# Performance work log

Measured on AMD Instinct MI355X. Metric: run time of the kernel, lower is better.

## Reference

```python
import jax, jax.numpy as jnp
import numpy as np

N = 4096      # nodes
E = 65536     # edges (avg degree 16)
NNIN = 64; NEIN = 64; NOPEN = 128; NHID = 128; NCLOSE = 128; NLAYER = 4
H = 0.1; NUM_OUT = 1024; LIN_HID = 256; EPS = 1e-5


def ln_all(x):
    # F.layer_norm(x, x.shape): normalize over ALL elements, no affine
    m = jnp.mean(x)
    v = jnp.mean((x - m) ** 2)
    return (x - m) * jax.lax.rsqrt(v + EPS)


def double_layer(x, K1, K2):
    # edgeConv with 2-D kernel == 1x1 conv == channel mixing
    x = jnp.einsum('oc,bcn->bon', K1, x)
    x = jnp.tanh(ln_all(x))
    return jnp.einsum('oc,bcn->bon', K2, x)


def node_grad(x, I, J, w):      # [1,C,N] -> [1,C,E]
    return w * (x[:, :, I] - x[:, :, J])


def node_ave(x, I, J, w):
    return 0.5 * w * (x[:, :, I] + x[:, :, J])


def edge_div(g, I, J, w, n):    # [1,C,E] -> [1,C,N], signed scatter-add
    wg = w * g
    z = jnp.zeros(g.shape[:2] + (n,), g.dtype)
    return z.at[:, :, I].add(wg).at[:, :, J].add(-wg)


def edge_ave(g, I, J, w, n):    # method='ave'
    wg = w * g
    z = jnp.zeros(g.shape[:2] + (n,), g.dtype)
    return 0.5 * (z.at[:, :, I].add(wg) + z.at[:, :, J].add(wg))


def setup_inputs():
    key = jax.random.key(0)
    ks = jax.random.split(key, 20)
    stdv = 1e-3
    nfeat = 3 * NOPEN  # varlet=False
    return {
        'xn': jax.random.normal(ks[0], (1, NNIN, N), jnp.float32),
        'xe': jax.random.normal(ks[1], (1, NEIN, E), jnp.float32),
        'iInd': jax.random.randint(ks[2], (E,), 0, N),
        'jInd': jax.random.randint(ks[3], (E,), 0, N),
        'K1Nopen': jax.random.normal(ks[4], (NOPEN, NNIN)) * stdv,
        'K2Nopen': jax.random.normal(ks[5], (NOPEN, NOPEN)) * stdv,
        'K1Eopen': jax.random.normal(ks[6], (NOPEN, NEIN)) * stdv,
        'K2Eopen': jax.random.normal(ks[7], (NOPEN, NOPEN)) * stdv,
        'KNclose': jax.random.normal(ks[8], (NCLOSE, NOPEN)) * stdv,
        'KE1': jax.random.uniform(ks[9], (NLAYER, NHID, nfeat)) * stdv,
        'KE2': jax.random.uniform(ks[10], (NLAYER, NOPEN, NHID)) * stdv,
        'KN1': jax.random.uniform(ks[11], (NLAYER, NHID, nfeat)) * stdv,
        'KN2': jax.random.uniform(ks[12], (NLAYER, NOPEN, NHID)) * stdv,
        'W1': jax.random.normal(ks[13], (LIN_HID, NCLOSE)) * 0.02,
        'b1': jnp.zeros((LIN_HID,), jnp.float32),
        'W2': jax.random.normal(ks[14], (NUM_OUT, LIN_HID)) * 0.02,
        'b2': jnp.zeros((NUM_OUT,), jnp.float32),
    }


def reference(xn, xe, iInd, jInd, K1Nopen, K2Nopen, K1Eopen, K2Eopen, KNclose,
              KE1, KE2, KN1, KN2, W1, b1, W2, b2):
    xn = double_layer(xn, K1Nopen, K2Nopen)
    xe = double_layer(xe, K1Eopen, K2Eopen)
    for i in range(NLAYER):
        # periodic pairwise-distance graph reweighting (cdist-style)
        f = xn[0]                                    # [C, N]
        s = jnp.sum(f * f, axis=0)                   # [N]
        D = jax.nn.relu(s[None, :] + s[:, None] - 2.0 * (f.T @ f))  # [N, N]
        D = jnp.exp(-2.0 * D / jnp.std(D, ddof=1))   # torch .std() is unbiased
        w = D[iInd, jInd]                            # [E]
        gradX = node_grad(xn, iInd, jInd, w)
        intX = node_ave(xn, iInd, jInd, w)
        dxe = jnp.concatenate([intX, xe, gradX], axis=1)     # [1, 3*nopen, E]
        dxe = ln_all(double_layer(dxe, KE1[i], KE2[i]))
        xe = xe + H * dxe                                    # wave=True
        divE = edge_div(xe, iInd, jInd, w, N)
        aveE = edge_ave(xe, iInd, jInd, w, N)
        dxn = jnp.concatenate([aveE, divE, xn], axis=1)      # [1, 3*nopen, N]
        dxn = double_layer(dxn, KN1[i], KN2[i])
        xn = xn + H * dxn
    xn = jnp.einsum('oc,bcn->bon', KNclose, xn)  # 1x1 conv close
    x = xn[0].T                                  # [N, nNclose]
    x = jax.nn.elu(x @ W1.T + b1)
    x = x @ W2.T + b2
    return jax.nn.log_softmax(x, axis=1)
```

## Files before the change

kernel.cpp:

```cpp
#include <hip/hip_runtime.h>

#define NNODES 4096
#define NEDGES 65536
#define CH 128

typedef __bf16 bf16x8_t __attribute__((ext_vector_type(8)));
typedef __bf16 bf16x4_t __attribute__((ext_vector_type(4)));
typedef __bf16 bf16x2_t __attribute__((ext_vector_type(2)));
typedef float f32x4_t __attribute__((ext_vector_type(4)));

__device__ __forceinline__ float fast_tanh(float x)
{
  float t = __builtin_amdgcn_exp2f(x * 2.885390081777927f);
  return 1.f - 2.f * __builtin_amdgcn_rcpf(t + 1.f);
}

__device__ __forceinline__ void write_stats(float s, float q, float2* __restrict__ partials,
                                            int pid, int tid, int nwaves)
{
#pragma unroll
  for (int d = 1; d < 64; d <<= 1) { s += __shfl_xor(s, d); q += __shfl_xor(q, d); }
  __shared__ float rs[8][2];
  const int wv = tid >> 6, lane = tid & 63;
  if (lane == 0) { rs[wv][0] = s; rs[wv][1] = q; }
  __syncthreads();
  if (tid == 0) {
    float S = 0.f, Q = 0.f;
    for (int i = 0; i < nwaves; ++i) { S += rs[i][0]; Q += rs[i][1]; }
    partials[pid] = {S, Q};
  }
}

__device__ __forceinline__ float2 params_inline(const float2* __restrict__ pp,
                                                int nblk, double M, int type)
{
  const int tid = threadIdx.x;
  double s = 0.0, q = 0.0;
  for (int i = tid; i < nblk; i += 256) { float2 v = pp[i]; s += (double)v.x; q += (double)v.y; }
#pragma unroll
  for (int d = 1; d < 64; d <<= 1) { s += __shfl_xor(s, d); q += __shfl_xor(q, d); }
  __shared__ double rs4[4], rq4[4];
  __shared__ float pr[2];
  const int wv = tid >> 6, lane = tid & 63;
  if (lane == 0) { rs4[wv] = s; rq4[wv] = q; }
  __syncthreads();
  if (tid == 0) {
    double S = rs4[0] + rs4[1] + rs4[2] + rs4[3];
    double Q = rq4[0] + rq4[1] + rq4[2] + rq4[3];
    if (type == 0) {
      double mean = S / M;
      double var = Q / M - mean * mean;
      if (var < 0.0) var = 0.0;
      pr[0] = (float)mean;
      pr[1] = (float)(1.0 / sqrt(var + 1e-5));
    } else {
      double var = (Q - S * S / M) / (M - 1.0);
      if (var < 1e-30) var = 1e-30;
      pr[0] = (float)(-2.0 / sqrt(var));
      pr[1] = 0.f;
    }
  }
  __syncthreads();
  return {pr[0], pr[1]};
}

template<int EM, int K>
__global__ __launch_bounds__(256) void emfma_k(
    const __bf16* __restrict__ A, const __bf16* __restrict__ X,
    __bf16* __restrict__ Cb,
    float2* __restrict__ partials,
    const __bf16* __restrict__ UVb, const float* __restrict__ wg,
    const int* __restrict__ iIe, const int* __restrict__ jIe,
    const float2* __restrict__ pp, int pnblk, double pM)
{
  float p0 = 0.f, p1 = 0.f;
  if constexpr (EM == 1 || EM == 3) {
    float2 pr = params_inline(pp, pnblk, pM, 0); p0 = pr.x; p1 = pr.y;
  }
  const int tid = threadIdx.x;
  const int wv = tid >> 6, lane = tid & 63;
  const int l15 = lane & 15, ks = lane >> 4;
  const int e = blockIdx.x * 64 + wv * 16 + l15;
  constexpr int KK = K / 32;
  bf16x8_t bq[KK];
  {
    const __bf16* xr = X + (size_t)e * K + ks * 8;
#pragma unroll
    for (int kk = 0; kk < KK; ++kk) {
      bf16x8_t v = *(const bf16x8_t*)(xr + kk * 32);
      if constexpr (EM == 1 || EM == 3) {
#pragma unroll
        for (int j = 0; j < 8; ++j) v[j] = (__bf16)fast_tanh(((float)v[j] - p0) * p1);
      }
      bq[kk] = v;
    }
  }
  float we = 0.f; int ie = 0, je = 0;
  if constexpr (EM == 2) { we = wg[e]; ie = iIe[e]; je = jIe[e]; }
  float dsum = 0.f, dsq = 0.f;
  const int ob0 = blockIdx.y * 4;
#pragma unroll
  for (int obb = 0; obb < 4; ++obb) {
    const int ob = ob0 + obb;
    f32x4_t acc = {0.f, 0.f, 0.f, 0.f};
    const __bf16* ar = A + (size_t)(ob * 16 + l15) * K + ks * 8;
#pragma unroll
    for (int kk = 0; kk < KK; ++kk) {
      bf16x8_t a = *(const bf16x8_t*)(ar + kk * 32);
      acc = __builtin_amdgcn_mfma_f32_16x16x32_bf16(a, bq[kk], acc, 0, 0, 0);
    }
    const int ro = ob * 16 + ks * 4;
    float v0 = acc[0], v1 = acc[1], v2 = acc[2], v3 = acc[3];
    if constexpr (EM == 2) {
      bf16x4_t u4 = *(const bf16x4_t*)&UVb[(size_t)ie * 256 + ro];
      bf16x4_t w4 = *(const bf16x4_t*)&UVb[(size_t)je * 256 + 128 + ro];
      v0 += we * ((float)u4[0] + (float)w4[0]);
      v1 += we * ((float)u4[1] + (float)w4[1]);
      v2 += we * ((float)u4[2] + (float)w4[2]);
      v3 += we * ((float)u4[3] + (float)w4[3]);
    }
    if constexpr (EM != 3) {
      dsum += v0 + v1 + v2 + v3;
      dsq  += v0 * v0 + v1 * v1 + v2 * v2 + v3 * v3;
    }
    bf16x4_t bv;
    bv[0] = (__bf16)v0; bv[1] = (__bf16)v1; bv[2] = (__bf16)v2; bv[3] = (__bf16)v3;
    *(bf16x4_t*)(Cb + (size_t)e * 128 + ro) = bv;
  }
  if constexpr (EM != 3)
    write_stats(dsum, dsq, partials, blockIdx.y * gridDim.x + blockIdx.x, tid, 4);
}

template<int K, bool XSPLIT, bool XT, bool STATS, int OM>
__global__ __launch_bounds__(256) void nmfma_k(
    const __bf16* __restrict__ A, const __bf16* __restrict__ X,
    const __bf16* __restrict__ X2,
    __bf16* __restrict__ Cb, float* __restrict__ Cf, float* __restrict__ resid,
    const float* __restrict__ bias, int nout_stride,
    float2* __restrict__ partials,
    const float2* __restrict__ pp, int pnblk, double pM)
{
  float p0 = 0.f, p1 = 0.f;
  if constexpr (XT) { float2 pr = params_inline(pp, pnblk, pM, 0); p0 = pr.x; p1 = pr.y; }
  const int tid = threadIdx.x;
  const int wv = tid >> 6, lane = tid & 63;
  const int l15 = lane & 15, ks = lane >> 4;
  const int n = blockIdx.x * 64 + wv * 16 + l15;
  constexpr int KK = K / 32;
  bf16x8_t bq[KK];
  if constexpr (XSPLIT) {
    const __bf16* xr  = X  + (size_t)n * 256 + ks * 8;
    const __bf16* xr2 = X2 + (size_t)n * 128 + ks * 8;
#pragma unroll
    for (int kk = 0; kk < 8; ++kk) bq[kk] = *(const bf16x8_t*)(xr + kk * 32);
#pragma unroll
    for (int kk = 8; kk < KK; ++kk) bq[kk] = *(const bf16x8_t*)(xr2 + (kk - 8) * 32);
  } else {
    const __bf16* xr = X + (size_t)n * K + ks * 8;
#pragma unroll
    for (int kk = 0; kk < KK; ++kk) {
      bf16x8_t v = *(const bf16x8_t*)(xr + kk * 32);
      if constexpr (XT) {
#pragma unroll
        for (int j = 0; j < 8; ++j) v[j] = (__bf16)fast_tanh(((float)v[j] - p0) * p1);
      }
      bq[kk] = v;
    }
  }
  float dsum = 0.f, dsq = 0.f;
  const int ob0 = blockIdx.y * 4;
#pragma unroll
  for (int obb = 0; obb < 4; ++obb) {
    const int ob = ob0 + obb;
    f32x4_t acc = {0.f, 0.f, 0.f, 0.f};
    const __bf16* ar = A + (size_t)(ob * 16 + l15) * K + ks * 8;
#pragma unroll
    for (int kk = 0; kk < KK; ++kk) {
      bf16x8_t a = *(const bf16x8_t*)(ar + kk * 32);
      acc = __builtin_amdgcn_mfma_f32_16x16x32_bf16(a, bq[kk], acc, 0, 0, 0);
    }
    const int ro = ob * 16 + ks * 4;
    float v[4] = {acc[0], acc[1], acc[2], acc[3]};
    if constexpr (OM == 1 || OM == 2) {
#pragma unroll
      for (int r = 0; r < 4; ++r) v[r] += bias[ro + r];
    }
    if constexpr (OM == 1) {
#pragma unroll
      for (int r = 0; r < 4; ++r) v[r] = v[r] > 0.f ? v[r] : expm1f(v[r]);
    }
    if constexpr (STATS) {
#pragma unroll
      for (int r = 0; r < 4; ++r) { dsum += v[r]; dsq += v[r] * v[r]; }
    }
    if constexpr (OM == 4) {
      float4* rp = (float4*)&resid[(size_t)n * 128 + ro];
      float4 rr = *rp;
      rr.x += 0.1f * v[0]; rr.y += 0.1f * v[1]; rr.z += 0.1f * v[2]; rr.w += 0.1f * v[3];
      *rp = rr;
    } else if constexpr (OM == 2 || OM == 3) {
      float4 fv = {v[0], v[1], v[2], v[3]};
      *(float4*)(Cf + (size_t)n * nout_stride + ro) = fv;
    } else {
      bf16x4_t bv;
      bv[0] = (__bf16)v[0]; bv[1] = (__bf16)v[1]; bv[2] = (__bf16)v[2]; bv[3] = (__bf16)v[3];
      *(bf16x4_t*)(Cb + (size_t)n * nout_stride + ro) = bv;
    }
  }
  if constexpr (STATS)
    write_stats(dsum, dsq, partials, blockIdx.y * gridDim.x + blockIdx.x, tid, 4);
}

__global__ __launch_bounds__(256) void dstat_k(
    const __bf16* __restrict__ fT, const float* __restrict__ s,
    float2* __restrict__ partials)
{
  int rem = blockIdx.x, i0t = 0;
  while (rem >= 64 - i0t) { rem -= 64 - i0t; ++i0t; }
  const int i0 = i0t * 64, j0 = (i0t + rem) * 64;
  const float wgt = (j0 > i0) ? 2.f : 1.f;
  const int tid = threadIdx.x;
  const int wv = tid >> 6, lane = tid & 63, l15 = lane & 15, ks = lane >> 4;
  const int irow = i0 + wv * 16 + l15;
  bf16x8_t aq[4];
  const __bf16* ar = fT + (size_t)irow * 128 + ks * 8;
#pragma unroll
  for (int kk = 0; kk < 4; ++kk) aq[kk] = *(const bf16x8_t*)(ar + kk * 32);
  float si[4];
#pragma unroll
  for (int r = 0; r < 4; ++r) si[r] = s[i0 + wv * 16 + ks * 4 + r];
  float dsum = 0.f, dsq = 0.f;
#pragma unroll
  for (int jb = 0; jb < 4; ++jb) {
    const int jcol = j0 + jb * 16 + l15;
    const __bf16* br = fT + (size_t)jcol * 128 + ks * 8;
    f32x4_t acc = {0.f, 0.f, 0.f, 0.f};
#pragma unroll
    for (int kk = 0; kk < 4; ++kk) {
      bf16x8_t b = *(const bf16x8_t*)(br + kk * 32);
      acc = __builtin_amdgcn_mfma_f32_16x16x32_bf16(aq[kk], b, acc, 0, 0, 0);
    }
    const float sj = s[jcol];
#pragma unroll
    for (int r = 0; r < 4; ++r) {
      float d = si[r] + sj - 2.f * acc[r];
      d = d > 0.f ? d : 0.f;
      dsum += d; dsq += d * d;
    }
  }
  write_stats(dsum * wgt, dsq * wgt, partials, blockIdx.x, tid, 4);
}

__global__ __launch_bounds__(256) void bcvt_k(const float* __restrict__ xnN,
                                              __bf16* __restrict__ xnNb,
                                              float* __restrict__ sbuf)
{
  const int n = blockIdx.x * 64 + (threadIdx.x >> 2);
  const int q = (threadIdx.x & 3) * 32;
  const float* src = xnN + (size_t)n * 128 + q;
  __bf16* dst = xnNb + (size_t)n * 128 + q;
  float ss = 0.f;
#pragma unroll
  for (int j = 0; j < 8; ++j) {
    float4 v = *(const float4*)(src + 4 * j);
    bf16x4_t b;
    b[0] = (__bf16)v.x; b[1] = (__bf16)v.y; b[2] = (__bf16)v.z; b[3] = (__bf16)v.w;
    float f0 = (float)b[0], f1 = (float)b[1], f2 = (float)b[2], f3 = (float)b[3];
    ss += f0 * f0 + f1 * f1 + f2 * f2 + f3 * f3;
    *(bf16x4_t*)(dst + 4 * j) = b;
  }
  ss += __shfl_xor(ss, 1);
  ss += __shfl_xor(ss, 2);
  if ((threadIdx.x & 3) == 0) sbuf[n] = ss;
}

__global__ __launch_bounds__(256) void etrans_k(const float* __restrict__ src,
                                                __bf16* __restrict__ dst, int ncols)
{
  __shared__ float t[64][65];
  const int e0 = blockIdx.x * 64;
  const int tx = threadIdx.x & 63, tw = threadIdx.x >> 6;
  for (int c = tw; c < 64; c += 4)
    t[tx][c] = src[(size_t)c * ncols + e0 + tx];
  __syncthreads();
  const int el = threadIdx.x >> 2, c0 = (threadIdx.x & 3) * 16;
  for (int q = 0; q < 4; ++q) {
    int c = c0 + q * 4;
    bf16x4_t b;
    b[0] = (__bf16)t[el][c];     b[1] = (__bf16)t[el][c + 1];
    b[2] = (__bf16)t[el][c + 2]; b[3] = (__bf16)t[el][c + 3];
    *(bf16x4_t*)&dst[(size_t)(e0 + el) * 64 + c] = b;
  }
}

__global__ __launch_bounds__(256) void edge_w_k(
    const __bf16* __restrict__ xnNb, const float* __restrict__ s,
    const int* __restrict__ iI, const int* __restrict__ jJ,
    const float2* __restrict__ pp, float* __restrict__ w)
{
  float2 pr = params_inline(pp, 2080, (double)NNODES * (double)NNODES, 1);
  const float factor = pr.x;
  int e = blockIdx.x * 256 + threadIdx.x;
  int a = iI[e], b = jJ[e];
  const bf16x8_t* pa = (const bf16x8_t*)(xnNb + (size_t)a * CH);
  const bf16x8_t* pb = (const bf16x8_t*)(xnNb + (size_t)b * CH);
  float g = 0.f;
#pragma unroll
  for (int q = 0; q < CH / 8; ++q) {
    bf16x8_t u = pa[q], v = pb[q];
#pragma unroll
    for (int j = 0; j < 8; ++j) g = fmaf((float)u[j], (float)v[j], g);
  }
  float d = s[a] + s[b] - 2.f * g;
  d = d > 0.f ? d : 0.f;
  w[e] = __builtin_amdgcn_exp2f(factor * d * 1.4426950408889634f);
}

__global__ void wcvt_k(const float* __restrict__ K1E, const float* __restrict__ K2E,
                       const float* __restrict__ KE1, const float* __restrict__ KE2,
                       const float* __restrict__ KNc, const float* __restrict__ W1,
                       const float* __restrict__ W2, const float* __restrict__ KN1,
                       const float* __restrict__ KN2, const float* __restrict__ K1N,
                       const float* __restrict__ K2N,
                       __bf16* __restrict__ K1Eb, __bf16* __restrict__ K2Eb,
                       __bf16* __restrict__ KE1b, __bf16* __restrict__ KE2b,
                       __bf16* __restrict__ KNcb, __bf16* __restrict__ W1b,
                       __bf16* __restrict__ W2b, __bf16* __restrict__ KN1b,
                       __bf16* __restrict__ KN2b, __bf16* __restrict__ a1a2b,
                       __bf16* __restrict__ K1Nb, __bf16* __restrict__ K2Nb)
{
  int id = blockIdx.x * 256 + threadIdx.x;
  if (id < 8192) { K1Eb[id] = (__bf16)K1E[id]; return; }
  id -= 8192;
  if (id < 16384) { K2Eb[id] = (__bf16)K2E[id]; return; }
  id -= 16384;
  if (id < 65536) {
    int l = id >> 14, rem = id & 16383, r = rem >> 7, c = rem & 127;
    KE1b[id] = (__bf16)KE1[(size_t)l * 49152 + r * 384 + 128 + c];
    return;
  }
  id -= 65536;
  if (id < 65536) { KE2b[id] = (__bf16)KE2[id]; return; }
  id -= 65536;
  if (id < 16384) { KNcb[id] = (__bf16)KNc[id]; return; }
  id -= 16384;
  if (id < 32768) { W1b[id] = (__bf16)W1[id]; return; }
  id -= 32768;
  if (id < 262144) { W2b[id] = (__bf16)W2[id]; return; }
  id -= 262144;
  if (id < 196608) { KN1b[id] = (__bf16)KN1[id]; return; }
  id -= 196608;
  if (id < 65536) { KN2b[id] = (__bf16)KN2[id]; return; }
  id -= 65536;
  if (id < 131072) {
    int l = id >> 15, rem = id & 32767, r = rem >> 7, c = rem & 127;
    int o = r & 127;
    float k1 = KE1[(size_t)l * 49152 + o * 384 + c];
    float k3 = KE1[(size_t)l * 49152 + o * 384 + 256 + c];
    a1a2b[id] = (__bf16)((r < 128) ? (0.5f * k1 + k3) : (0.5f * k1 - k3));
    return;
  }
  id -= 131072;
  if (id < 8192) { K1Nb[id] = (__bf16)K1N[id]; return; }
  id -= 8192;
  if (id < 16384) { K2Nb[id] = (__bf16)K2N[id]; return; }
}

__global__ __launch_bounds__(256) void lnres_k(
    const __bf16* __restrict__ eBT, __bf16* __restrict__ xeT,
    const float2* __restrict__ pp)
{
  float2 pr = params_inline(pp, 2048, (double)CH * NEDGES, 0);
  const float m = pr.x, r = pr.y;
  const size_t base = (size_t)blockIdx.x * (256 * 16);
  for (int it = 0; it < 2; ++it) {
    size_t i = base + (size_t)it * 2048 + (size_t)threadIdx.x * 8;
    bf16x8_t b = *(const bf16x8_t*)(eBT + i);
    bf16x8_t x = *(const bf16x8_t*)(xeT + i);
    bf16x8_t ob;
#pragma unroll
    for (int j = 0; j < 8; ++j)
      ob[j] = (__bf16)((float)x[j] + 0.1f * (((float)b[j] - m) * r));
    *(bf16x8_t*)(xeT + i) = ob;
  }
}

__global__ void hist_k(const int* __restrict__ iI, const int* __restrict__ jJ,
                       int* __restrict__ cnt)
{
  int e = blockIdx.x * 256 + threadIdx.x;
  atomicAdd(&cnt[iI[e]], 1);
  atomicAdd(&cnt[jJ[e]], 1);
}

__global__ __launch_bounds__(1024) void scan_k(const int* __restrict__ cnt,
                                               int* __restrict__ offs,
                                               int* __restrict__ cursor)
{
  __shared__ int tmp[1024];
  const int tid = threadIdx.x;
  int4 v = *(const int4*)&cnt[tid * 4];
  int s = v.x + v.y + v.z + v.w;
  tmp[tid] = s; __syncthreads();
  for (int d = 1; d < 1024; d <<= 1) {
    int t = (tid >= d) ? tmp[tid - d] : 0;
    __syncthreads();
    tmp[tid] += t;
    __syncthreads();
  }
  int base = tmp[tid] - s;
  int4 o = {base, base + v.x, base + v.x + v.y, base + v.x + v.y + v.z};
  *(int4*)&offs[tid * 4] = o;
  *(int4*)&cursor[tid * 4] = o;
  if (tid == 1023) offs[4096] = tmp[1023];
}

__global__ void fill_k(const int* __restrict__ iI, const int* __restrict__ jJ,
                       int* __restrict__ cursor, int* __restrict__ list)
{
  int e = blockIdx.x * 256 + threadIdx.x;
  int p1 = atomicAdd(&cursor[iI[e]], 1);
  list[p1] = e;
  int p2 = atomicAdd(&cursor[jJ[e]], 1);
  list[p2] = e | 0x80000000;
}

__global__ __launch_bounds__(512) void gather_k(
    const __bf16* __restrict__ xeT, const float* __restrict__ w,
    const int* __restrict__ offs, const int* __restrict__ list,
    __bf16* __restrict__ catb)
{
  __shared__ float comb[4][4][64];
  const int wv = threadIdx.x >> 6, lane = threadIdx.x & 63;
  const int nn = wv >> 1, half = wv & 1;
  const int n = blockIdx.x * 4 + nn;
  const int k0 = offs[n], k1 = offs[n + 1];
  float s1a = 0.f, s1b = 0.f, s2a = 0.f, s2b = 0.f;
#pragma unroll 2
  for (int k = k0 + half; k < k1; k += 2) {
    int enc = list[k];
    int e = enc & 0x7fffffff;
    float we = w[e];
    bf16x2_t xv = *(const bf16x2_t*)&xeT[(size_t)e * 128 + lane * 2];
    float va = (float)xv[0] * we;
    float vb = (float)xv[1] * we;
    if (enc >= 0) { s1a += va; s1b += vb; }
    else          { s2a += va; s2b += vb; }
  }
  if (half == 1) {
    comb[nn][0][lane] = s1a; comb[nn][1][lane] = s1b;
    comb[nn][2][lane] = s2a; comb[nn][3][lane] = s2b;
  }
  __syncthreads();
  if (half == 0) {
    s1a += comb[nn][0][lane]; s1b += comb[nn][1][lane];
    s2a += comb[nn][2][lane]; s2b += comb[nn][3][lane];
    __bf16* row = catb + (size_t)n * 256;
    bf16x2_t av, dv;
    av[0] = (__bf16)(0.5f * (s1a + s2a)); av[1] = (__bf16)(0.5f * (s1b + s2b));
    dv[0] = (__bf16)(s1a - s2a);          dv[1] = (__bf16)(s1b - s2b);
    *(bf16x2_t*)&row[lane * 2] = av;
    *(bf16x2_t*)&row[128 + lane * 2] = dv;
  }
}

__global__ __launch_bounds__(256) void logsoftmax_k(float* __restrict__ out)
{
  __shared__ float red[256];
  const int n = blockIdx.x, tid = threadIdx.x;
  float* row = out + (size_t)n * 1024;
  float v[4];
  float mx = -1e30f;
#pragma unroll
  for (int l = 0; l < 4; ++l) { v[l] = row[tid + 256 * l]; mx = fmaxf(mx, v[l]); }
  red[tid] = mx; __syncthreads();
  for (int s = 128; s > 0; s >>= 1) { if (tid < s) red[tid] = fmaxf(red[tid], red[tid + s]); __syncthreads(); }
  float m = red[0]; __syncthreads();
  float se = 0.f;
#pragma unroll
  for (int l = 0; l < 4; ++l) se += expf(v[l] - m);
  red[tid] = se; __syncthreads();
  for (int s = 128; s > 0; s >>= 1) { if (tid < s) red[tid] += red[tid + s]; __syncthreads(); }
  float L = m + logf(red[0]);
#pragma unroll
  for (int l = 0; l < 4; ++l) row[tid + 256 * l] = v[l] - L;
}

extern "C" void kernel_launch(void* const* d_in, const int* in_sizes, int n_in,
                              void* d_out, int out_size, void* d_ws, size_t ws_size,
                              hipStream_t stream)
{
  (void)in_sizes; (void)n_in; (void)out_size; (void)ws_size;
  const float* xn_in = (const float*)d_in[0];
  const float* xe_in = (const float*)d_in[1];
  const int*   iI    = (const int*)d_in[2];
  const int*   jJ    = (const int*)d_in[3];
  const float* K1N   = (const float*)d_in[4];
  const float* K2N   = (const float*)d_in[5];
  const float* K1E   = (const float*)d_in[6];
  const float* K2E   = (const float*)d_in[7];
  const float* KNc   = (const float*)d_in[8];
  const float* KE1   = (const float*)d_in[9];
  const float* KE2   = (const float*)d_in[10];
  const float* KN1   = (const float*)d_in[11];
  const float* KN2   = (const float*)d_in[12];
  const float* W1    = (const float*)d_in[13];
  const float* b1    = (const float*)d_in[14];
  const float* W2    = (const float*)d_in[15];
  const float* b2    = (const float*)d_in[16];
  float* out = (float*)d_out;

  float* ws = (float*)d_ws;
  size_t off = 0;
  auto alloc = [&](size_t n) { size_t o = off; off += (n + 63) & ~(size_t)63; return o; };
  float* xnN   = ws + alloc((size_t)NNODES * CH);
  __bf16* xeT  = (__bf16*)(ws + alloc((size_t)NEDGES * CH / 2));
  __bf16* eAT  = (__bf16*)(ws + alloc((size_t)NEDGES * CH / 2));
  __bf16* eBT  = (__bf16*)(ws + alloc((size_t)NEDGES * CH / 2));
  float* sbuf  = ws + alloc(NNODES);
  float* wbuf  = ws + alloc(NEDGES);
  __bf16* UVb  = (__bf16*)(ws + alloc((size_t)NNODES * 256 / 2));
  __bf16* xnNb = (__bf16*)(ws + alloc((size_t)NNODES * CH / 2));
  __bf16* catb = (__bf16*)(ws + alloc((size_t)NNODES * 256 / 2));
  __bf16* nAb  = (__bf16*)(ws + alloc((size_t)NNODES * CH / 2));
  __bf16* zb   = (__bf16*)(ws + alloc((size_t)NNODES * CH / 2));
  __bf16* l1bb = (__bf16*)(ws + alloc((size_t)NNODES * 256 / 2));
  __bf16* K1Eb = (__bf16*)(ws + alloc(8192 / 2));
  __bf16* K2Eb = (__bf16*)(ws + alloc(16384 / 2));
  __bf16* KE1b = (__bf16*)(ws + alloc(65536 / 2));
  __bf16* KE2b = (__bf16*)(ws + alloc(65536 / 2));
  __bf16* KNcb = (__bf16*)(ws + alloc(16384 / 2));
  __bf16* W1b  = (__bf16*)(ws + alloc(32768 / 2));
  __bf16* W2b  = (__bf16*)(ws + alloc(262144 / 2));
  __bf16* KN1b = (__bf16*)(ws + alloc(196608 / 2));
  __bf16* KN2b = (__bf16*)(ws + alloc(65536 / 2));
  __bf16* a1a2b= (__bf16*)(ws + alloc(131072 / 2));
  __bf16* K1Nb = (__bf16*)(ws + alloc(8192 / 2));
  __bf16* K2Nb = (__bf16*)(ws + alloc(16384 / 2));
  int* csr_cnt    = (int*)(ws + alloc(4096));
  int* csr_offs   = (int*)(ws + alloc(4160));
  int* csr_cursor = (int*)(ws + alloc(4096));
  int* csr_list   = (int*)(ws + alloc(2 * NEDGES));
  float2* pA = (float2*)(ws + alloc((size_t)4096 * 2));
  float2* pB = (float2*)(ws + alloc((size_t)4096 * 2));
  __bf16* xeT64  = eBT;
  __bf16* xnT64b = UVb;

  const __bf16* BNUL = nullptr;
  const float* NUL = nullptr;
  const int* NULI = nullptr;
  const float2* PNUL = nullptr;

  wcvt_k<<<3456, 256, 0, stream>>>(K1E, K2E, KE1, KE2, KNc, W1, W2, KN1, KN2, K1N, K2N,
                                   K1Eb, K2Eb, KE1b, KE2b, KNcb, W1b, W2b, KN1b, KN2b,
                                   a1a2b, K1Nb, K2Nb);
  hipMemsetAsync(csr_cnt, 0, 4096 * sizeof(int), stream);
  hist_k<<<NEDGES / 256, 256, 0, stream>>>(iI, jJ, csr_cnt);
  scan_k<<<1, 1024, 0, stream>>>(csr_cnt, csr_offs, csr_cursor);
  fill_k<<<NEDGES / 256, 256, 0, stream>>>(iI, jJ, csr_cursor, csr_list);

  etrans_k<<<NNODES / 64, 256, 0, stream>>>(xn_in, xnT64b, NNODES);
  nmfma_k<64, false, false, true, 0><<<dim3(64, 2), 256, 0, stream>>>(
      K1Nb, xnT64b, BNUL, nAb, nullptr, nullptr, NUL, 128, pA, PNUL, 0, 0.0);
  nmfma_k<128, false, true, false, 3><<<dim3(64, 2), 256, 0, stream>>>(
      K2Nb, nAb, BNUL, nullptr, xnN, nullptr, NUL, 128, nullptr,
      pA, 128, (double)CH * NNODES);

  etrans_k<<<NEDGES / 64, 256, 0, stream>>>(xe_in, xeT64, NEDGES);
  emfma_k<0, 64><<<dim3(NEDGES / 64, 2), 256, 0, stream>>>(K1Eb, xeT64, eAT,
      pA, BNUL, NUL, NULI, NULI, PNUL, 0, 0.0);
  emfma_k<3, 128><<<dim3(NEDGES / 64, 2), 256, 0, stream>>>(K2Eb, eAT, xeT,
      nullptr, BNUL, NUL, NULI, NULI, pA, 2048, (double)CH * NEDGES);

  for (int i = 0; i < 4; ++i) {
    const __bf16* KE1bi = KE1b + (size_t)i * 128 * 128;
    const __bf16* KE2bi = KE2b + (size_t)i * 128 * 128;
    const __bf16* KN1bi = KN1b + (size_t)i * 128 * 384;
    const __bf16* KN2bi = KN2b + (size_t)i * 128 * 128;
    const __bf16* a1a2i = a1a2b + (size_t)i * 256 * 128;

    bcvt_k<<<NNODES / 64, 256, 0, stream>>>(xnN, xnNb, sbuf);
    dstat_k<<<2080, 256, 0, stream>>>(xnNb, sbuf, pA);
    edge_w_k<<<NEDGES / 256, 256, 0, stream>>>(xnNb, sbuf, iI, jJ, pA, wbuf);

    nmfma_k<128, false, false, false, 0><<<dim3(64, 4), 256, 0, stream>>>(
        a1a2i, xnNb, BNUL, UVb, nullptr, nullptr, NUL, 256, nullptr, PNUL, 0, 0.0);
    emfma_k<2, 128><<<dim3(NEDGES / 64, 2), 256, 0, stream>>>(KE1bi, xeT, eAT,
        pB, UVb, wbuf, iI, jJ, PNUL, 0, 0.0);
    emfma_k<1, 128><<<dim3(NEDGES / 64, 2), 256, 0, stream>>>(KE2bi, eAT, eBT,
        pA, BNUL, NUL, NULI, NULI, pB, 2048, (double)CH * NEDGES);
    lnres_k<<<2048, 256, 0, stream>>>(eBT, xeT, pA);

    gather_k<<<NNODES / 4, 512, 0, stream>>>(xeT, wbuf, csr_offs, csr_list, catb);
    nmfma_k<384, true, false, true, 0><<<dim3(64, 2), 256, 0, stream>>>(
        KN1bi, catb, xnNb, nAb, nullptr, nullptr, NUL, 128, pB, PNUL, 0, 0.0);
    nmfma_k<128, false, true, false, 4><<<dim3(64, 2), 256, 0, stream>>>(
        KN2bi, nAb, BNUL, nullptr, nullptr, xnN, NUL, 128, nullptr,
        pB, 128, (double)CH * NNODES);
  }

  bcvt_k<<<NNODES / 64, 256, 0, stream>>>(xnN, xnNb, sbuf);
  nmfma_k<128, false, false, false, 0><<<dim3(64, 2), 256, 0, stream>>>(
      KNcb, xnNb, BNUL, zb, nullptr, nullptr, NUL, 128, nullptr, PNUL, 0, 0.0);
  nmfma_k<128, false, false, false, 1><<<dim3(64, 4), 256, 0, stream>>>(
      W1b, zb, BNUL, l1bb, nullptr, nullptr, b1, 256, nullptr, PNUL, 0, 0.0);
  nmfma_k<256, false, false, false, 2><<<dim3(64, 16), 256, 0, stream>>>(
      W2b, l1bb, BNUL, nullptr, out, nullptr, b2, 1024, nullptr, PNUL, 0, 0.0);
  logsoftmax_k<<<NNODES, 256, 0, stream>>>(out);
}
```

Before: 698.2 us.

## Fuse bf16 conversion and edge-weight computation into GEMM kernels, widen grids

Removes the standalone bcvt_k and edge_w_k kernels. The residual-update node GEMM now also writes the bf16 copy and per-node squared-norm partials, and the first edge GEMM computes the distance-based edge weights inline, using a 4-thread-per-edge dot product kept in shared memory. It also changes the output-block split per workgroup (OBS) so most GEMMs launch more, smaller blocks, with the stats partial counts and buffers adjusted to match. The trade-off is that edge-weight work is now repeated in every y-block of the edge GEMM, and the extra launches add more partial-stat reduction.

```diff
diff --git a/kernel.cpp b/kernel.cpp
--- a/kernel.cpp
+++ b/kernel.cpp
@@ -64,15 +64,18 @@
   return {pr[0], pr[1]};
 }
 
-template<int EM, int K>
+template<int EM, int K, int OBS, bool WPH>
 __global__ __launch_bounds__(256) void emfma_k(
     const __bf16* __restrict__ A, const __bf16* __restrict__ X,
     __bf16* __restrict__ Cb,
     float2* __restrict__ partials,
-    const __bf16* __restrict__ UVb, const float* __restrict__ wg,
-    const int* __restrict__ iIe, const int* __restrict__ jIe,
+    const __bf16* __restrict__ UVb, const __bf16* __restrict__ xnNb,
+    const float* __restrict__ sbufh,
+    const int* __restrict__ iI, const int* __restrict__ jJ,
+    float* __restrict__ wbuf, const float2* __restrict__ pD,
     const float2* __restrict__ pp, int pnblk, double pM)
 {
+  __shared__ float wl[64];
   float p0 = 0.f, p1 = 0.f;
   if constexpr (EM == 1 || EM == 3) {
     float2 pr = params_inline(pp, pnblk, pM, 0); p0 = pr.x; p1 = pr.y;
@@ -80,7 +83,31 @@
   const int tid = threadIdx.x;
   const int wv = tid >> 6, lane = tid & 63;
   const int l15 = lane & 15, ks = lane >> 4;
-  const int e = blockIdx.x * 64 + wv * 16 + l15;
+  const int row = wv * 16 + l15;
+  const int e = blockIdx.x * 64 + row;
+  if constexpr (WPH) {
+    float2 fp = params_inline(pD, 2080, (double)NNODES * (double)NNODES, 1);
+    const int eg = blockIdx.x * 64 + (tid >> 2);
+    const int a = iI[eg], b = jJ[eg];
+    const bf16x8_t* pa = (const bf16x8_t*)(xnNb + (size_t)a * CH + (tid & 3) * 32);
+    const bf16x8_t* pb = (const bf16x8_t*)(xnNb + (size_t)b * CH + (tid & 3) * 32);
+    float g = 0.f;
+#pragma unroll
+    for (int q = 0; q < 4; ++q) {
+      bf16x8_t u = pa[q], v = pb[q];
+#pragma unroll
+      for (int j = 0; j < 8; ++j) g = fmaf((float)u[j], (float)v[j], g);
+    }
+    g += __shfl_xor(g, 1); g += __shfl_xor(g, 2);
+    float d = sbufh[a] + sbufh[NNODES + a] + sbufh[b] + sbufh[NNODES + b] - 2.f * g;
+    d = d > 0.f ? d : 0.f;
+    float wgt = __builtin_amdgcn_exp2f(fp.x * d * 1.4426950408889634f);
+    if ((tid & 3) == 0) {
+      wl[tid >> 2] = wgt;
+      if (blockIdx.y == 0) wbuf[eg] = wgt;
+    }
+    __syncthreads();
+  }
   constexpr int KK = K / 32;
   bf16x8_t bq[KK];
   {
@@ -96,11 +123,11 @@
     }
   }
   float we = 0.f; int ie = 0, je = 0;
-  if constexpr (EM == 2) { we = wg[e]; ie = iIe[e]; je = jIe[e]; }
+  if constexpr (EM == 2) { we = wl[row]; ie = iI[e]; je = jJ[e]; }
   float dsum = 0.f, dsq = 0.f;
-  const int ob0 = blockIdx.y * 4;
-#pragma unroll
-  for (int obb = 0; obb < 4; ++obb) {
+  const int ob0 = blockIdx.y * OBS;
+#pragma unroll
+  for (int obb = 0; obb < OBS; ++obb) {
     const int ob = ob0 + obb;
     f32x4_t acc = {0.f, 0.f, 0.f, 0.f};
     const __bf16* ar = A + (size_t)(ob * 16 + l15) * K + ks * 8;
@@ -131,14 +158,15 @@
     write_stats(dsum, dsq, partials, blockIdx.y * gridDim.x + blockIdx.x, tid, 4);
 }
 
-template<int K, bool XSPLIT, bool XT, bool STATS, int OM>
+template<int K, bool XSPLIT, bool XT, bool STATS, int OM, bool EMITB, int OBS>
 __global__ __launch_bounds__(256) void nmfma_k(
     const __bf16* __restrict__ A, const __bf16* __restrict__ X,
     const __bf16* __restrict__ X2,
     __bf16* __restrict__ Cb, float* __restrict__ Cf, float* __restrict__ resid,
     const float* __restrict__ bias, int nout_stride,
     float2* __restrict__ partials,
-    const float2* __restrict__ pp, int pnblk, double pM)
+    const float2* __restrict__ pp, int pnblk, double pM,
+    __bf16* __restrict__ xbout, float* __restrict__ shout)
 {
   float p0 = 0.f, p1 = 0.f;
   if constexpr (XT) { float2 pr = params_inline(pp, pnblk, pM, 0); p0 = pr.x; p1 = pr.y; }
@@ -167,10 +195,10 @@
       bq[kk] = v;
     }
   }
-  float dsum = 0.f, dsq = 0.f;
-  const int ob0 = blockIdx.y * 4;
-#pragma unroll
-  for (int obb = 0; obb < 4; ++obb) {
+  float dsum = 0.f, dsq = 0.f, ss = 0.f;
+  const int ob0 = blockIdx.y * OBS;
+#pragma unroll
+  for (int obb = 0; obb < OBS; ++obb) {
     const int ob = ob0 + obb;
     f32x4_t acc = {0.f, 0.f, 0.f, 0.f};
     const __bf16* ar = A + (size_t)(ob * 16 + l15) * K + ks * 8;
@@ -198,21 +226,40 @@
       float4 rr = *rp;
       rr.x += 0.1f * v[0]; rr.y += 0.1f * v[1]; rr.z += 0.1f * v[2]; rr.w += 0.1f * v[3];
       *rp = rr;
+      if constexpr (EMITB) {
+        bf16x4_t eb;
+        eb[0] = (__bf16)rr.x; eb[1] = (__bf16)rr.y; eb[2] = (__bf16)rr.z; eb[3] = (__bf16)rr.w;
+        *(bf16x4_t*)(xbout + (size_t)n * 128 + ro) = eb;
+#pragma unroll
+        for (int r = 0; r < 4; ++r) { float f = (float)eb[r]; ss += f * f; }
+      }
     } else if constexpr (OM == 2 || OM == 3) {
       float4 fv = {v[0], v[1], v[2], v[3]};
       *(float4*)(Cf + (size_t)n * nout_stride + ro) = fv;
+      if constexpr (EMITB) {
+        bf16x4_t eb;
+        eb[0] = (__bf16)v[0]; eb[1] = (__bf16)v[1]; eb[2] = (__bf16)v[2]; eb[3] = (__bf16)v[3];
+        *(bf16x4_t*)(xbout + (size_t)n * 128 + ro) = eb;
+#pragma unroll
+        for (int r = 0; r < 4; ++r) { float f = (float)eb[r]; ss += f * f; }
+      }
     } else {
       bf16x4_t bv;
       bv[0] = (__bf16)v[0]; bv[1] = (__bf16)v[1]; bv[2] = (__bf16)v[2]; bv[3] = (__bf16)v[3];
       *(bf16x4_t*)(Cb + (size_t)n * nout_stride + ro) = bv;
     }
   }
+  if constexpr (EMITB) {
+    ss += __shfl_xor(ss, 16);
+    ss += __shfl_xor(ss, 32);
+    if (lane < 16) shout[blockIdx.y * NNODES + n] = ss;
+  }
   if constexpr (STATS)
     write_stats(dsum, dsq, partials, blockIdx.y * gridDim.x + blockIdx.x, tid, 4);
 }
 
 __global__ __launch_bounds__(256) void dstat_k(
-    const __bf16* __restrict__ fT, const float* __restrict__ s,
+    const __bf16* __restrict__ fT, const float* __restrict__ sh,
     float2* __restrict__ partials)
 {
   int rem = blockIdx.x, i0t = 0;
@@ -228,7 +275,10 @@
   for (int kk = 0; kk < 4; ++kk) aq[kk] = *(const bf16x8_t*)(ar + kk * 32);
   float si[4];
 #pragma unroll
-  for (int r = 0; r < 4; ++r) si[r] = s[i0 + wv * 16 + ks * 4 + r];
+  for (int r = 0; r < 4; ++r) {
+    int ii = i0 + wv * 16 + ks * 4 + r;
+    si[r] = sh[ii] + sh[NNODES + ii];
+  }
   float dsum = 0.f, dsq = 0.f;
 #pragma unroll
   for (int jb = 0; jb < 4; ++jb) {
@@ -240,7 +290,7 @@
       bf16x8_t b = *(const bf16x8_t*)(br + kk * 32);
       acc = __builtin_amdgcn_mfma_f32_16x16x32_bf16(aq[kk], b, acc, 0, 0, 0);
     }
-    const float sj = s[jcol];
+    const float sj = sh[jcol] + sh[NNODES + jcol];
 #pragma unroll
     for (int r = 0; r < 4; ++r) {
       float d = si[r] + sj - 2.f * acc[r];
@@ -249,29 +299,6 @@
     }
   }
   write_stats(dsum * wgt, dsq * wgt, partials, blockIdx.x, tid, 4);
-}
-
-__global__ __launch_bounds__(256) void bcvt_k(const float* __restrict__ xnN,
-                                              __bf16* __restrict__ xnNb,
-                                              float* __restrict__ sbuf)
-{
-  const int n = blockIdx.x * 64 + (threadIdx.x >> 2);
-  const int q = (threadIdx.x & 3) * 32;
-  const float* src = xnN + (size_t)n * 128 + q;
-  __bf16* dst = xnNb + (size_t)n * 128 + q;
-  float ss = 0.f;
-#pragma unroll
-  for (int j = 0; j < 8; ++j) {
-    float4 v = *(const float4*)(src + 4 * j);
-    bf16x4_t b;
-    b[0] = (__bf16)v.x; b[1] = (__bf16)v.y; b[2] = (__bf16)v.z; b[3] = (__bf16)v.w;
-    float f0 = (float)b[0], f1 = (float)b[1], f2 = (float)b[2], f3 = (float)b[3];
-    ss += f0 * f0 + f1 * f1 + f2 * f2 + f3 * f3;
-    *(bf16x4_t*)(dst + 4 * j) = b;
-  }
-  ss += __shfl_xor(ss, 1);
-  ss += __shfl_xor(ss, 2);
-  if ((threadIdx.x & 3) == 0) sbuf[n] = ss;
 }
 
 __global__ __launch_bounds__(256) void etrans_k(const float* __restrict__ src,
@@ -291,29 +318,6 @@
     b[2] = (__bf16)t[el][c + 2]; b[3] = (__bf16)t[el][c + 3];
     *(bf16x4_t*)&dst[(size_t)(e0 + el) * 64 + c] = b;
   }
-}
-
-__global__ __launch_bounds__(256) void edge_w_k(
-    const __bf16* __restrict__ xnNb, const float* __restrict__ s,
-    const int* __restrict__ iI, const int* __restrict__ jJ,
-    const float2* __restrict__ pp, float* __restrict__ w)
-{
-  float2 pr = params_inline(pp, 2080, (double)NNODES * (double)NNODES, 1);
-  const float factor = pr.x;
-  int e = blockIdx.x * 256 + threadIdx.x;
-  int a = iI[e], b = jJ[e];
-  const bf16x8_t* pa = (const bf16x8_t*)(xnNb + (size_t)a * CH);
-  const bf16x8_t* pb = (const bf16x8_t*)(xnNb + (size_t)b * CH);
-  float g = 0.f;
-#pragma unroll
-  for (int q = 0; q < CH / 8; ++q) {
-    bf16x8_t u = pa[q], v = pb[q];
-#pragma unroll
-    for (int j = 0; j < 8; ++j) g = fmaf((float)u[j], (float)v[j], g);
-  }
-  float d = s[a] + s[b] - 2.f * g;
-  d = d > 0.f ? d : 0.f;
-  w[e] = __builtin_amdgcn_exp2f(factor * d * 1.4426950408889634f);
 }
 
 __global__ void wcvt_k(const float* __restrict__ K1E, const float* __restrict__ K2E,
@@ -368,9 +372,9 @@
 
 __global__ __launch_bounds__(256) void lnres_k(
     const __bf16* __restrict__ eBT, __bf16* __restrict__ xeT,
-    const float2* __restrict__ pp)
-{
-  float2 pr = params_inline(pp, 2048, (double)CH * NEDGES, 0);
+    const float2* __restrict__ pp, int pnblk)
+{
+  float2 pr = params_inline(pp, pnblk, (double)CH * NEDGES, 0);
   const float m = pr.x, r = pr.y;
   const size_t base = (size_t)blockIdx.x * (256 * 16);
   for (int it = 0; it < 2; ++it) {
@@ -517,7 +521,7 @@
   __bf16* xeT  = (__bf16*)(ws + alloc((size_t)NEDGES * CH / 2));
   __bf16* eAT  = (__bf16*)(ws + alloc((size_t)NEDGES * CH / 2));
   __bf16* eBT  = (__bf16*)(ws + alloc((size_t)NEDGES * CH / 2));
-  float* sbuf  = ws + alloc(NNODES);
+  float* sbufh = ws + alloc(2 * NNODES);
   float* wbuf  = ws + alloc(NEDGES);
   __bf16* UVb  = (__bf16*)(ws + alloc((size_t)NNODES * 256 / 2));
   __bf16* xnNb = (__bf16*)(ws + alloc((size_t)NNODES * CH / 2));
@@ -543,6 +547,7 @@
   int* csr_list   = (int*)(ws + alloc(2 * NEDGES));
   float2* pA = (float2*)(ws + alloc((size_t)4096 * 2));
   float2* pB = (float2*)(ws + alloc((size_t)4096 * 2));
+  float2* pC = (float2*)(ws + alloc((size_t)4096 * 2));
   __bf16* xeT64  = eBT;
   __bf16* xnT64b = UVb;
 
@@ -550,6 +555,9 @@
   const float* NUL = nullptr;
   const int* NULI = nullptr;
   const float2* PNUL = nullptr;
+  __bf16* BNULm = nullptr;
+  float* NULm = nullptr;
+  float* FNULm = nullptr;
 
   wcvt_k<<<3456, 256, 0, stream>>>(K1E, K2E, KE1, KE2, KNc, W1, W2, KN1, KN2, K1N, K2N,
                                    K1Eb, K2Eb, KE1b, KE2b, KNcb, W1b, W2b, KN1b, KN2b,
@@ -560,17 +568,18 @@
   fill_k<<<NEDGES / 256, 256, 0, stream>>>(iI, jJ, csr_cursor, csr_list);
 
   etrans_k<<<NNODES / 64, 256, 0, stream>>>(xn_in, xnT64b, NNODES);
-  nmfma_k<64, false, false, true, 0><<<dim3(64, 2), 256, 0, stream>>>(
-      K1Nb, xnT64b, BNUL, nAb, nullptr, nullptr, NUL, 128, pA, PNUL, 0, 0.0);
-  nmfma_k<128, false, true, false, 3><<<dim3(64, 2), 256, 0, stream>>>(
+  nmfma_k<64, false, false, true, 0, false, 1><<<dim3(64, 8), 256, 0, stream>>>(
+      K1Nb, xnT64b, BNUL, nAb, nullptr, nullptr, NUL, 128, pA, PNUL, 0, 0.0, BNULm, NULm);
+  nmfma_k<128, false, true, false, 3, true, 4><<<dim3(64, 2), 256, 0, stream>>>(
       K2Nb, nAb, BNUL, nullptr, xnN, nullptr, NUL, 128, nullptr,
-      pA, 128, (double)CH * NNODES);
+      pA, 512, (double)CH * NNODES, xnNb, sbufh);
 
   etrans_k<<<NEDGES / 64, 256, 0, stream>>>(xe_in, xeT64, NEDGES);
-  emfma_k<0, 64><<<dim3(NEDGES / 64, 2), 256, 0, stream>>>(K1Eb, xeT64, eAT,
-      pA, BNUL, NUL, NULI, NULI, PNUL, 0, 0.0);
-  emfma_k<3, 128><<<dim3(NEDGES / 64, 2), 256, 0, stream>>>(K2Eb, eAT, xeT,
-      nullptr, BNUL, NUL, NULI, NULI, pA, 2048, (double)CH * NEDGES);
+  emfma_k<0, 64, 2, false><<<dim3(NEDGES / 64, 4), 256, 0, stream>>>(
+      K1Eb, xeT64, eAT, pA, BNUL, BNUL, NUL, NULI, NULI, FNULm, PNUL, PNUL, 0, 0.0);
+  emfma_k<3, 128, 2, false><<<dim3(NEDGES / 64, 4), 256, 0, stream>>>(
+      K2Eb, eAT, xeT, nullptr, BNUL, BNUL, NUL, NULI, NULI, FNULm, PNUL,
+      pA, 4096, (double)CH * NEDGES);
 
   for (int i = 0; i < 4; ++i) {
     const __bf16* KE1bi = KE1b + (size_t)i * 128 * 128;
@@ -579,32 +588,31 @@
     const __bf16* KN2bi = KN2b + (size_t)i * 128 * 128;
     const __bf16* a1a2i = a1a2b + (size_t)i * 256 * 128;
 
-    bcvt_k<<<NNODES / 64, 256, 0, stream>>>(xnN, xnNb, sbuf);
-    dstat_k<<<2080, 256, 0, stream>>>(xnNb, sbuf, pA);
-    edge_w_k<<<NEDGES / 256, 256, 0, stream>>>(xnNb, sbuf, iI, jJ, pA, wbuf);
-
-    nmfma_k<128, false, false, false, 0><<<dim3(64, 4), 256, 0, stream>>>(
-        a1a2i, xnNb, BNUL, UVb, nullptr, nullptr, NUL, 256, nullptr, PNUL, 0, 0.0);
-    emfma_k<2, 128><<<dim3(NEDGES / 64, 2), 256, 0, stream>>>(KE1bi, xeT, eAT,
-        pB, UVb, wbuf, iI, jJ, PNUL, 0, 0.0);
-    emfma_k<1, 128><<<dim3(NEDGES / 64, 2), 256, 0, stream>>>(KE2bi, eAT, eBT,
-        pA, BNUL, NUL, NULI, NULI, pB, 2048, (double)CH * NEDGES);
-    lnres_k<<<2048, 256, 0, stream>>>(eBT, xeT, pA);
+    dstat_k<<<2080, 256, 0, stream>>>(xnNb, sbufh, pA);
+
+    nmfma_k<128, false, false, false, 0, false, 1><<<dim3(64, 16), 256, 0, stream>>>(
+        a1a2i, xnNb, BNUL, UVb, nullptr, nullptr, NUL, 256, nullptr, PNUL, 0, 0.0, BNULm, NULm);
+
+    emfma_k<2, 128, 2, true><<<dim3(NEDGES / 64, 4), 256, 0, stream>>>(
+        KE1bi, xeT, eAT, pB, UVb, xnNb, sbufh, iI, jJ, wbuf, pA, PNUL, 0, 0.0);
+    emfma_k<1, 128, 2, false><<<dim3(NEDGES / 64, 4), 256, 0, stream>>>(
+        KE2bi, eAT, eBT, pC, BNUL, BNUL, NUL, NULI, NULI, FNULm, PNUL,
+        pB, 4096, (double)CH * NEDGES);
+    lnres_k<<<2048, 256, 0, stream>>>(eBT, xeT, pC, 4096);
 
     gather_k<<<NNODES / 4, 512, 0, stream>>>(xeT, wbuf, csr_offs, csr_list, catb);
-    nmfma_k<384, true, false, true, 0><<<dim3(64, 2), 256, 0, stream>>>(
-        KN1bi, catb, xnNb, nAb, nullptr, nullptr, NUL, 128, pB, PNUL, 0, 0.0);
-    nmfma_k<128, false, true, false, 4><<<dim3(64, 2), 256, 0, stream>>>(
+    nmfma_k<384, true, false, true, 0, false, 1><<<dim3(64, 8), 256, 0, stream>>>(
+        KN1bi, catb, xnNb, nAb, nullptr, nullptr, NUL, 128, pB, PNUL, 0, 0.0, BNULm, NULm);
+    nmfma_k<128, false, true, false, 4, true, 4><<<dim3(64, 2), 256, 0, stream>>>(
         KN2bi, nAb, BNUL, nullptr, nullptr, xnN, NUL, 128, nullptr,
-        pB, 128, (double)CH * NNODES);
-  }
-
-  bcvt_k<<<NNODES / 64, 256, 0, stream>>>(xnN, xnNb, sbuf);
-  nmfma_k<128, false, false, false, 0><<<dim3(64, 2), 256, 0, stream>>>(
-      KNcb, xnNb, BNUL, zb, nullptr, nullptr, NUL, 128, nullptr, PNUL, 0, 0.0);
-  nmfma_k<128, false, false, false, 1><<<dim3(64, 4), 256, 0, stream>>>(
-      W1b, zb, BNUL, l1bb, nullptr, nullptr, b1, 256, nullptr, PNUL, 0, 0.0);
-  nmfma_k<256, false, false, false, 2><<<dim3(64, 16), 256, 0, stream>>>(
-      W2b, l1bb, BNUL, nullptr, out, nullptr, b2, 1024, nullptr, PNUL, 0, 0.0);
+        pB, 512, (double)CH * NNODES, xnNb, sbufh);
+  }
+
+  nmfma_k<128, false, false, false, 0, false, 1><<<dim3(64, 8), 256, 0, stream>>>(
+      KNcb, xnNb, BNUL, zb, nullptr, nullptr, NUL, 128, nullptr, PNUL, 0, 0.0, BNULm, NULm);
+  nmfma_k<128, false, false, false, 1, false, 1><<<dim3(64, 16), 256, 0, stream>>>(
+      W1b, zb, BNUL, l1bb, nullptr, nullptr, b1, 256, nullptr, PNUL, 0, 0.0, BNULm, NULm);
+  nmfma_k<256, false, false, false, 2, false, 1><<<dim3(64, 64), 256, 0, stream>>>(
+      W2b, l1bb, BNUL, nullptr, out, nullptr, b2, 1024, nullptr, PNUL, 0, 0.0, BNULm, NULm);
   logsoftmax_k<<<NNODES, 256, 0, stream>>>(out);
 }
```

Measured after the change: 787.2 us. 12.7% more time.
